# Optimization experiments

Hardware: AMD Instinct MI355X
Metric: run time of the kernel (lower is better)

Reference implementation:

```python
import jax, jax.numpy as jnp
import numpy as np

B, N, E, F, FE, H = 4, 1024, 65536, 96, 32, 12
DH = F // H
EPS = 1e-3  # keras LayerNormalization default epsilon


def layer_norm(x, g, b):
    m = jnp.mean(x, axis=-1, keepdims=True)
    v = jnp.var(x, axis=-1, keepdims=True)
    return (x - m) / jnp.sqrt(v + EPS) * g + b


def setup_inputs() -> dict:
    key = jax.random.key(0)
    ks = jax.random.split(key, 14)
    s = lambda d: 1.0 / np.sqrt(d)
    return {
        "nodes": jax.random.normal(ks[0], (B, N, F), jnp.float32),
        "edge_features": jax.random.normal(ks[1], (B, E, FE), jnp.float32),
        "distance": jax.random.uniform(ks[2], (B, E, 1), jnp.float32),
        "edges": jax.random.randint(ks[3], (B, E, 2), 0, N, jnp.int32),
        # message MLP: Dense(2F+FE -> F) + GELU + LayerNorm
        "Wm": jax.random.normal(ks[4], (2 * F + FE, F), jnp.float32) * s(2 * F + FE),
        "bm": jnp.zeros((F,), jnp.float32),
        "g1": jnp.ones((F,), jnp.float32),
        "b1": jnp.zeros((F,), jnp.float32),
        # gated multi-head self-attention over concat([nodes, aggregated]) (2F -> F)
        "Wq": jax.random.normal(ks[5], (2 * F, F), jnp.float32) * s(2 * F),
        "bq": jnp.zeros((F,), jnp.float32),
        "Wk": jax.random.normal(ks[6], (2 * F, F), jnp.float32) * s(2 * F),
        "bk": jnp.zeros((F,), jnp.float32),
        "Wv": jax.random.normal(ks[7], (2 * F, F), jnp.float32) * s(2 * F),
        "bv": jnp.zeros((F,), jnp.float32),
        "Wg": jax.random.normal(ks[8], (2 * F, F), jnp.float32) * s(2 * F),
        "bg": jnp.zeros((F,), jnp.float32),
        "Wo": jax.random.normal(ks[9], (F, F), jnp.float32) * s(F),
        "bo": jnp.zeros((F,), jnp.float32),
        "g2": jnp.ones((F,), jnp.float32),
        "b2": jnp.zeros((F,), jnp.float32),
        # learnable gaussian edge-weight params
        "sigma": jnp.full((1,), 0.005, jnp.float32),
        "beta": jnp.full((1,), 4.0, jnp.float32),
    }


def reference(nodes, edge_features, distance, edges, Wm, bm, g1, b1,
              Wq, bq, Wk, bk, Wv, bv, Wg, bg, Wo, bo, g2, b2, sigma, beta):
    # --- message: gather endpoint node features per edge ---
    gathered = jax.vmap(lambda n, e: n[e])(nodes, edges)              # [B,E,2,F]
    msg_in = jnp.concatenate([gathered.reshape(B, E, 2 * F), edge_features], axis=-1)
    messages = layer_norm(jax.nn.gelu(msg_in @ Wm + bm, approximate=False), g1, b1)  # [B,E,F]
    # --- learnable gaussian edge weighting ---
    edge_weights = jnp.exp(-((distance ** 2 / (2.0 * sigma ** 2)) ** beta))           # [B,E,1]
    weighted_messages = messages * edge_weights
    # --- scatter: per-graph segment-sum into receiver nodes (edge[:,1]) ---
    aggregated = jax.vmap(lambda m, seg: jax.ops.segment_sum(m, seg, num_segments=N))(
        weighted_messages, edges[..., 1])                             # [B,N,F]
    # --- update: gated multi-head self-attention on concat([nodes, aggregated]) ---
    x = jnp.concatenate([nodes, aggregated], axis=-1)                 # [B,N,2F]
    heads = lambda t: t.reshape(B, N, H, DH).transpose(0, 2, 1, 3)    # [B,H,N,DH]
    q, k, v = heads(x @ Wq + bq), heads(x @ Wk + bk), heads(x @ Wv + bv)
    gate = heads(jax.nn.sigmoid(x @ Wg + bg))
    attn = jax.nn.softmax(jnp.einsum("bhqd,bhkd->bhqk", q, k) / jnp.sqrt(jnp.float32(DH)), axis=-1)
    out = (jnp.einsum("bhqk,bhkd->bhqd", attn, v) * gate).transpose(0, 2, 1, 3).reshape(B, N, F)
    out = out @ Wo + bo
    updated_nodes = layer_norm(jax.nn.gelu(out, approximate=False), g2, b2)
    return (updated_nodes, weighted_messages, distance, edges)
```

## Files before the change

kernel.cpp:

```cpp
#include <hip/hip_runtime.h>
#include <math.h>

#define Bn 4
#define Nn 1024
#define En 65536
#define Fn 96
#define FEn 32
#define Hn 12

#define OUT_UPD  0
#define OUT_WM   393216LL
#define OUT_DIST 25559040LL
#define OUT_EDGE 25821184LL

#define WS_AGG  0
#define WS_Q    393216
#define WS_K    786432
#define WS_V    1179648
#define WS_G    1572864
#define WS_AO   1966080
#define WS_LIST 2359296
#define WS_LW   2424832
#define WS_CNT  2490368

#define MSG_NWAVES 1024

__device__ __forceinline__ float gelu_exact(float x) {
    return 0.5f * x * (1.0f + erff(x * 0.70710678118654752f));
}

__device__ __forceinline__ void zero_wm_chunk(int c, const float* __restrict__ dist,
                                              const float* __restrict__ sigma,
                                              const float* __restrict__ beta,
                                              float* __restrict__ out_wm,
                                              int tid, int nthr, int* s_act) {
    if (tid < 256) {
        int ge = c * 256 + tid;
        float d = dist[ge];
        float sg = sigma[0], bt = beta[0];
        float t = d * d / (2.0f * sg * sg);
        s_act[tid] = (powf(t, bt) < 90.0f) ? 1 : 0;
    }
    __syncthreads();
    const float4 z = make_float4(0.f, 0.f, 0.f, 0.f);
    float4* wm4 = (float4*)out_wm + (size_t)c * 6144;
    for (int p = tid; p < 6144; p += nthr) {
        if (!s_act[p / 24]) wm4[p] = z;
    }
}

__global__ void zero_kernel(float* __restrict__ agg, int* __restrict__ gcnt) {
    int i = blockIdx.x * 256 + threadIdx.x;
    const float4 z = make_float4(0.f, 0.f, 0.f, 0.f);
    float4* p = (float4*)agg;
    p[i] = z;
    p[i + 49152] = z;
    if (i == 0) gcnt[0] = 0;
}

__global__ __launch_bounds__(1024) void scan_kernel(
        const float* __restrict__ dist, const int* __restrict__ edges,
        const float* __restrict__ sigma, const float* __restrict__ beta,
        float* __restrict__ out_dist, float* __restrict__ out_edges,
        int* __restrict__ glist, float* __restrict__ gw,
        int* __restrict__ gcnt) {
    __shared__ int wcnt[16], wbase[16], blkbase;
    int tid = threadIdx.x;
    int lane = tid & 63, wv = tid >> 6;
    int ge = blockIdx.x * 1024 + tid;
    float d = dist[ge];
    out_dist[ge] = d;
    int e0 = edges[2 * ge], e1 = edges[2 * ge + 1];
    *(float2*)&out_edges[2 * ge] = make_float2((float)e0, (float)e1);
    float sg = sigma[0], bt = beta[0];
    float t  = d * d / (2.0f * sg * sg);
    float tp = powf(t, bt);
    bool active = (tp < 90.0f);
    float w = active ? expf(-tp) : 0.0f;

    unsigned long long mask = __ballot(active);
    int lp = __popcll(mask & ((1ull << lane) - 1ull));
    if (lane == 0) wcnt[wv] = __popcll(mask);
    __syncthreads();
    if (tid == 0) {
        int a = 0;
        #pragma unroll
        for (int i = 0; i < 16; ++i) { wbase[i] = a; a += wcnt[i]; }
        blkbase = a ? atomicAdd(gcnt, a) : 0;
    }
    __syncthreads();
    if (active) {
        int pos = blkbase + wbase[wv] + lp;
        if (pos < 65536) { glist[pos] = ge; gw[pos] = w; }
    }
}

__global__ __launch_bounds__(256) void msg_kernel(
        const int* __restrict__ glist, const float* __restrict__ gw,
        const int* __restrict__ gcnt, const int* __restrict__ edges,
        const float* __restrict__ nodes, const float* __restrict__ ef,
        const float* __restrict__ Wm, const float* __restrict__ bm,
        const float* __restrict__ g1, const float* __restrict__ b1,
        float* __restrict__ out_wm, float* __restrict__ agg) {
    __shared__ float sin_s[4][4][232];
    int tid = threadIdx.x;
    int lane = tid & 63, wv = tid >> 6;
    int count = gcnt[0];
    if (count > 65536) count = 65536;
    int c2 = 64 + (lane & 31);
    int wid = blockIdx.x * 4 + wv;

    for (int base = wid * 4; base < count; base += MSG_NWAVES * 4) {
        int   gei[4];
        float wgt[4];
        bool  val[4];
        #pragma unroll
        for (int e = 0; e < 4; ++e) {
            int ai = base + e;
            val[e] = (ai < count);
            int as = val[e] ? ai : base;
            gei[e] = glist[as];
            wgt[e] = val[e] ? gw[ai] : 0.0f;
        }
        #pragma unroll
        for (int e = 0; e < 4; ++e) {
            int g = gei[e];
            int b = g >> 16;
            int e0 = edges[2 * g], e1 = edges[2 * g + 1];
            const float* n0 = nodes + ((size_t)b * Nn + e0) * 96;
            const float* n1 = nodes + ((size_t)b * Nn + e1) * 96;
            const float* ep = ef + (size_t)g * 32;
            #pragma unroll
            for (int ii = 0; ii < 4; ++ii) {
                int i = ii * 64 + lane;
                if (i < 224) {
                    float v = (i < 96) ? n0[i] : (i < 192) ? n1[i - 96] : ep[i - 192];
                    sin_s[wv][e][i] = v;
                }
            }
        }
        float acc[4][2];
        #pragma unroll
        for (int e = 0; e < 4; ++e) { acc[e][0] = bm[lane]; acc[e][1] = bm[c2]; }
        #pragma unroll 8
        for (int i = 0; i < 224; ++i) {
            float w1 = Wm[i * 96 + lane];
            float w2 = Wm[i * 96 + c2];
            #pragma unroll
            for (int e = 0; e < 4; ++e) {
                float a = sin_s[wv][e][i];
                acc[e][0] = fmaf(a, w1, acc[e][0]);
                acc[e][1] = fmaf(a, w2, acc[e][1]);
            }
        }
        #pragma unroll
        for (int e = 0; e < 4; ++e) {
            if (!val[e]) continue;
            float y1 = gelu_exact(acc[e][0]);
            float y2 = gelu_exact(acc[e][1]);
            float c2v = (lane < 32) ? y2 : 0.0f;
            float sum  = y1 + c2v;
            float sum2 = y1 * y1 + c2v * c2v;
            #pragma unroll
            for (int off = 1; off < 64; off <<= 1) {
                sum  += __shfl_xor(sum, off);
                sum2 += __shfl_xor(sum2, off);
            }
            float mean = sum * (1.0f / 96.0f);
            float var  = sum2 * (1.0f / 96.0f) - mean * mean;
            float rs   = rsqrtf(var + 1e-3f);
            int g = gei[e];
            int b = g >> 16;
            int e1 = edges[2 * g + 1];
            float* aggp = agg + ((size_t)b * Nn + e1) * 96;
            float* wmp  = out_wm + (size_t)g * 96;
            float o1 = ((y1 - mean) * rs * g1[lane] + b1[lane]) * wgt[e];
            wmp[lane] = o1;
            atomicAdd(&aggp[lane], o1);
            if (lane < 32) {
                float o2 = ((y2 - mean) * rs * g1[c2] + b1[c2]) * wgt[e];
                wmp[c2] = o2;
                atomicAdd(&aggp[c2], o2);
            }
        }
    }
}

__global__ void proj_kernel(const float* __restrict__ nodes, const float* __restrict__ agg,
                            const float* __restrict__ Wq, const float* __restrict__ bq,
                            const float* __restrict__ Wk, const float* __restrict__ bk,
                            const float* __restrict__ Wv, const float* __restrict__ bv,
                            const float* __restrict__ Wg, const float* __restrict__ bg,
                            float* __restrict__ qo, float* __restrict__ ko,
                            float* __restrict__ vo, float* __restrict__ go,
                            const float* __restrict__ dist, const float* __restrict__ sigma,
                            const float* __restrict__ beta, float* __restrict__ out_wm) {
    __shared__ float xs[32][200];
    __shared__ float Wt[64 * 96];
    __shared__ int s_act[256];
    int tid = threadIdx.x;
    int m = blockIdx.y;
    if (m == 0) {
        zero_wm_chunk(768 + blockIdx.x, dist, sigma, beta, out_wm, tid, 256, s_act);
    }
    const float* W    = (m == 0) ? Wq : (m == 1) ? Wk : (m == 2) ? Wv : Wg;
    const float* bias = (m == 0) ? bq : (m == 1) ? bk : (m == 2) ? bv : bg;
    float* outp       = (m == 0) ? qo : (m == 1) ? ko : (m == 2) ? vo : go;
    int row0 = blockIdx.x * 32;
    int b = row0 >> 10, n0 = row0 & 1023;
    for (int i = tid; i < 32 * 192; i += 256) {
        int r = i / 192, k = i % 192;
        size_t row = row0 + r;
        xs[r][k] = (k < 96) ? nodes[row * 96 + k] : agg[row * 96 + (k - 96)];
    }
    int rg = tid >> 4;
    int cg = tid & 15;
    float acc[12];
    #pragma unroll
    for (int c = 0; c < 12; ++c) acc[c] = 0.0f;
    for (int kc = 0; kc < 3; ++kc) {
        __syncthreads();
        {
            float4* Wt4 = (float4*)Wt;
            const float4* Wg4 = (const float4*)(W + kc * 64 * 96);
            for (int i = tid; i < 1536; i += 256) Wt4[i] = Wg4[i];
        }
        __syncthreads();
        #pragma unroll 4
        for (int k = 0; k < 64; ++k) {
            float a0 = xs[rg * 2 + 0][kc * 64 + k];
            float a1 = xs[rg * 2 + 1][kc * 64 + k];
            #pragma unroll
            for (int c = 0; c < 6; ++c) {
                float wv_ = Wt[k * 96 + cg * 6 + c];
                acc[c]     = fmaf(a0, wv_, acc[c]);
                acc[6 + c] = fmaf(a1, wv_, acc[6 + c]);
            }
        }
    }
    #pragma unroll
    for (int i = 0; i < 2; ++i) {
        #pragma unroll
        for (int c = 0; c < 6; ++c) {
            int col = cg * 6 + c;
            float v = acc[i * 6 + c] + bias[col];
            if (m == 3) v = 1.0f / (1.0f + expf(-v));
            xs[rg * 2 + i][col] = v;
        }
    }
    __syncthreads();
    float4* out4 = (float4*)outp;
    for (int j = tid; j < 768; j += 256) {
        int h = j >> 6, idx = j & 63;
        int r = idx >> 1, half = idx & 1;
        float4 v = *(const float4*)&xs[r][h * 8 + half * 4];
        out4[(((size_t)b * Hn + h) * Nn + n0) * 2 + idx] = v;
    }
}

__global__ __launch_bounds__(512, 6) void attn_kernel(
        const float* __restrict__ qp, const float* __restrict__ kp,
        const float* __restrict__ vp, const float* __restrict__ gp,
        float* __restrict__ ao,
        const float* __restrict__ dist, const float* __restrict__ sigma,
        const float* __restrict__ beta, float* __restrict__ out_wm) {
    __shared__ float sl[512];
    __shared__ float sacc[512][9];
    __shared__ int s_act[256];
    int tid = threadIdx.x;
    zero_wm_chunk(blockIdx.y * 16 + blockIdx.x, dist, sigma, beta, out_wm, tid, 512, s_act);
    int bh = blockIdx.y;
    int lane = tid & 63;
    int w = __builtin_amdgcn_readfirstlane(tid >> 6);
    int n = blockIdx.x * 64 + lane;
    size_t hb = (size_t)bh * (Nn * 8);
    size_t qoff = hb + (size_t)n * 8;

    const float scale = 0.35355339059327376f;
    float4 q0 = *(const float4*)&qp[qoff];
    float4 q1 = *(const float4*)&qp[qoff + 4];
    q0.x *= scale; q0.y *= scale; q0.z *= scale; q0.w *= scale;
    q1.x *= scale; q1.y *= scale; q1.z *= scale; q1.w *= scale;

    const float4* kc4 = (const float4*)(kp + hb) + (size_t)w * 256;
    const float4* vc4 = (const float4*)(vp + hb) + (size_t)w * 256;

    float l = 0.0f;
    float a0 = 0, a1 = 0, a2 = 0, a3 = 0, a4 = 0, a5 = 0, a6 = 0, a7 = 0;
    for (int g = 0; g < 32; ++g) {
        float4 T[8];
        #pragma unroll
        for (int i = 0; i < 8; ++i) T[i] = kc4[g * 8 + i];
        float s[4];
        #pragma unroll
        for (int jj = 0; jj < 4; ++jj) {
            float4 k0 = T[jj * 2], k1 = T[jj * 2 + 1];
            s[jj] = q0.x * k0.x + q0.y * k0.y + q0.z * k0.z + q0.w * k0.w +
                    q1.x * k1.x + q1.y * k1.y + q1.z * k1.z + q1.w * k1.w;
        }
        #pragma unroll
        for (int i = 0; i < 8; ++i) T[i] = vc4[g * 8 + i];
        float p[4];
        #pragma unroll
        for (int jj = 0; jj < 4; ++jj) p[jj] = __expf(s[jj]);
        l += (p[0] + p[1]) + (p[2] + p[3]);
        #pragma unroll
        for (int jj = 0; jj < 4; ++jj) {
            float4 v0 = T[jj * 2], v1 = T[jj * 2 + 1];
            a0 = fmaf(p[jj], v0.x, a0);  a1 = fmaf(p[jj], v0.y, a1);
            a2 = fmaf(p[jj], v0.z, a2);  a3 = fmaf(p[jj], v0.w, a3);
            a4 = fmaf(p[jj], v1.x, a4);  a5 = fmaf(p[jj], v1.y, a5);
            a6 = fmaf(p[jj], v1.z, a6);  a7 = fmaf(p[jj], v1.w, a7);
        }
    }
    sl[tid] = l;
    sacc[tid][0] = a0; sacc[tid][1] = a1; sacc[tid][2] = a2; sacc[tid][3] = a3;
    sacc[tid][4] = a4; sacc[tid][5] = a5; sacc[tid][6] = a6; sacc[tid][7] = a7;
    __syncthreads();
    if (tid < 64) {
        float L = 0.0f;
        float o[8] = {0, 0, 0, 0, 0, 0, 0, 0};
        #pragma unroll
        for (int i = 0; i < 8; ++i) {
            L += sl[tid + 64 * i];
            #pragma unroll
            for (int d = 0; d < 8; ++d)
                o[d] += sacc[tid + 64 * i][d];
        }
        float invL = 1.0f / L;
        float4 g0 = *(const float4*)&gp[qoff];
        float4 g1v = *(const float4*)&gp[qoff + 4];
        float4 r0 = make_float4(o[0] * invL * g0.x, o[1] * invL * g0.y,
                                o[2] * invL * g0.z, o[3] * invL * g0.w);
        float4 r1 = make_float4(o[4] * invL * g1v.x, o[5] * invL * g1v.y,
                                o[6] * invL * g1v.z, o[7] * invL * g1v.w);
        *(float4*)&ao[qoff] = r0;
        *(float4*)&ao[qoff + 4] = r1;
    }
}

__global__ __launch_bounds__(512) void out_kernel(
        const float* __restrict__ ao, const float* __restrict__ Wo,
        const float* __restrict__ bo, const float* __restrict__ g2,
        const float* __restrict__ b2, float* __restrict__ out0,
        const float* __restrict__ dist, const float* __restrict__ sigma,
        const float* __restrict__ beta, float* __restrict__ out_wm) {
    __shared__ float Wsh[96 * 96];
    __shared__ float as_[32][104];
    __shared__ int s_act[256];
    int tid = threadIdx.x;
    zero_wm_chunk(896 + blockIdx.x, dist, sigma, beta, out_wm, tid, 512, s_act);
    int row0 = blockIdx.x * 32;
    int b = row0 >> 10, n0 = row0 & 1023;
    {
        float4* W4 = (float4*)Wsh;
        const float4* Wg4 = (const float4*)Wo;
        for (int i = tid; i < 2304; i += 512) W4[i] = Wg4[i];
    }
    const float4* ao4 = (const float4*)ao;
    for (int j = tid; j < 768; j += 512) {
        int h = j >> 6, idx = j & 63;
        int r = idx >> 1, half = idx & 1;
        float4 v = ao4[(((size_t)b * Hn + h) * Nn + n0) * 2 + idx];
        *(float4*)&as_[r][h * 8 + half * 4] = v;
    }
    __syncthreads();
    int r = tid >> 4, cg = tid & 15;
    float acc[6];
    #pragma unroll
    for (int c = 0; c < 6; ++c) acc[c] = 0.0f;
    for (int k = 0; k < 96; ++k) {
        float a = as_[r][k];
        #pragma unroll
        for (int c = 0; c < 6; ++c)
            acc[c] = fmaf(a, Wsh[k * 96 + cg * 6 + c], acc[c]);
    }
    float yv[6];
    float sum = 0.0f, sum2 = 0.0f;
    #pragma unroll
    for (int c = 0; c < 6; ++c) {
        float t = acc[c] + bo[cg * 6 + c];
        float g = gelu_exact(t);
        yv[c] = g;
        sum += g; sum2 += g * g;
    }
    #pragma unroll
    for (int off = 1; off < 16; off <<= 1) {
        sum  += __shfl_xor(sum, off);
        sum2 += __shfl_xor(sum2, off);
    }
    float mean = sum * (1.0f / 96.0f);
    float var  = sum2 * (1.0f / 96.0f) - mean * mean;
    float rs   = rsqrtf(var + 1e-3f);
    size_t row = row0 + r;
    #pragma unroll
    for (int c = 0; c < 6; ++c)
        out0[row * 96 + cg * 6 + c] = (yv[c] - mean) * rs * g2[cg * 6 + c] + b2[cg * 6 + c];
}

extern "C" void kernel_launch(void* const* d_in, const int* in_sizes, int n_in,
                              void* d_out, int out_size, void* d_ws, size_t ws_size,
                              hipStream_t stream) {
    const float* nodes = (const float*)d_in[0];
    const float* ef    = (const float*)d_in[1];
    const float* dist  = (const float*)d_in[2];
    const int*   edges = (const int*)d_in[3];
    const float* Wm = (const float*)d_in[4];
    const float* bm = (const float*)d_in[5];
    const float* g1 = (const float*)d_in[6];
    const float* b1 = (const float*)d_in[7];
    const float* Wq = (const float*)d_in[8];
    const float* bq = (const float*)d_in[9];
    const float* Wk = (const float*)d_in[10];
    const float* bk = (const float*)d_in[11];
    const float* Wv = (const float*)d_in[12];
    const float* bv = (const float*)d_in[13];
    const float* Wg = (const float*)d_in[14];
    const float* bg = (const float*)d_in[15];
    const float* Wo = (const float*)d_in[16];
    const float* bo = (const float*)d_in[17];
    const float* g2 = (const float*)d_in[18];
    const float* b2 = (const float*)d_in[19];
    const float* sigma = (const float*)d_in[20];
    const float* beta  = (const float*)d_in[21];

    float* out = (float*)d_out;
    float* ws  = (float*)d_ws;

    float* agg  = ws + WS_AGG;
    float* qb   = ws + WS_Q;
    float* kb   = ws + WS_K;
    float* vb   = ws + WS_V;
    float* gwb  = ws + WS_G;
    float* aob  = ws + WS_AO;
    int*   glist = (int*)(ws + WS_LIST);
    float* glw   = ws + WS_LW;
    int*   gcnt  = (int*)(ws + WS_CNT);

    zero_kernel<<<192, 256, 0, stream>>>(agg, gcnt);

    scan_kernel<<<Bn * En / 1024, 1024, 0, stream>>>(
        dist, edges, sigma, beta, out + OUT_DIST, out + OUT_EDGE, glist, glw, gcnt);

    msg_kernel<<<256, 256, 0, stream>>>(
        glist, glw, gcnt, edges, nodes, ef, Wm, bm, g1, b1, out + OUT_WM, agg);

    dim3 gp_(128, 4);
    proj_kernel<<<gp_, 256, 0, stream>>>(
        nodes, agg, Wq, bq, Wk, bk, Wv, bv, Wg, bg, qb, kb, vb, gwb,
        dist, sigma, beta, out + OUT_WM);

    dim3 ga(16, Bn * Hn);
    attn_kernel<<<ga, 512, 0, stream>>>(qb, kb, vb, gwb, aob,
                                        dist, sigma, beta, out + OUT_WM);

    out_kernel<<<Bn * Nn / 32, 512, 0, stream>>>(aob, Wo, bo, g2, b2, out + OUT_UPD,
                                                 dist, sigma, beta, out + OUT_WM);
}
```

Measured before the change: 113.9 us.

## Rewrite attention kernel with bf16 MFMA and LDS-staged K/V

Replaces the scalar fp32 per-query attention loop with a bf16 MFMA formulation. K and a transposed V are converted to bf16 and staged in shared memory, with a row of ones appended to V so the softmax denominator comes out of the same MFMA. Each wave processes 16 queries over 32-key chunks, passing probabilities through LDS between the two MFMAs. This cuts the FP32 ALU work and the redundant global K/V reads, at the cost of bf16 precision in scores and probabilities, no max subtraction, and a per-block staging of the full K/V into LDS.

```diff
diff --git a/kernel.cpp b/kernel.cpp
--- a/kernel.cpp
+++ b/kernel.cpp
@@ -25,8 +25,17 @@
 
 #define MSG_NWAVES 1024
 
+typedef __attribute__((ext_vector_type(8))) short bf16x8;
+typedef __attribute__((ext_vector_type(4))) float f32x4;
+
 __device__ __forceinline__ float gelu_exact(float x) {
     return 0.5f * x * (1.0f + erff(x * 0.70710678118654752f));
+}
+
+__device__ __forceinline__ unsigned cvtpk_bf16(float lo, float hi) {
+    unsigned r;
+    asm("v_cvt_pk_bf16_f32 %0, %1, %2" : "=v"(r) : "v"(lo), "v"(hi));
+    return r;
 }
 
 __device__ __forceinline__ void zero_wm_chunk(int c, const float* __restrict__ dist,
@@ -258,84 +267,92 @@
     }
 }
 
-__global__ __launch_bounds__(512, 6) void attn_kernel(
+__global__ __launch_bounds__(256, 4) void attn_kernel(
         const float* __restrict__ qp, const float* __restrict__ kp,
         const float* __restrict__ vp, const float* __restrict__ gp,
         float* __restrict__ ao,
         const float* __restrict__ dist, const float* __restrict__ sigma,
         const float* __restrict__ beta, float* __restrict__ out_wm) {
-    __shared__ float sl[512];
-    __shared__ float sacc[512][9];
+    __shared__ __align__(16) unsigned short K_s[1024][8];
+    __shared__ __align__(16) unsigned short Vt_s[9][1032];
+    __shared__ __align__(16) unsigned short P_s[4][16][32];
     __shared__ int s_act[256];
     int tid = threadIdx.x;
-    zero_wm_chunk(blockIdx.y * 16 + blockIdx.x, dist, sigma, beta, out_wm, tid, 512, s_act);
+    zero_wm_chunk(blockIdx.y * 16 + blockIdx.x, dist, sigma, beta, out_wm, tid, 256, s_act);
+
     int bh = blockIdx.y;
-    int lane = tid & 63;
-    int w = __builtin_amdgcn_readfirstlane(tid >> 6);
-    int n = blockIdx.x * 64 + lane;
+    int lane = tid & 63, wv = tid >> 6;
     size_t hb = (size_t)bh * (Nn * 8);
-    size_t qoff = hb + (size_t)n * 8;
+    const float* kc = kp + hb;
+    const float* vc = vp + hb;
+
+    {
+        const float2* k2 = (const float2*)kc;
+        unsigned* kw = (unsigned*)&K_s[0][0];
+        for (int i = tid; i < 4096; i += 256) {
+            float2 v = k2[i];
+            kw[i] = cvtpk_bf16(v.x, v.y);
+        }
+    }
+    for (int i = tid; i < 8192; i += 256) {
+        float v = vc[i];
+        int k = i >> 3, n = i & 7;
+        Vt_s[n][k] = (unsigned short)cvtpk_bf16(v, v);
+    }
+    {
+        unsigned* ow = (unsigned*)&Vt_s[8][0];
+        for (int i = tid; i < 516; i += 256) ow[i] = 0x3F803F80u;
+    }
 
     const float scale = 0.35355339059327376f;
-    float4 q0 = *(const float4*)&qp[qoff];
-    float4 q1 = *(const float4*)&qp[qoff + 4];
-    q0.x *= scale; q0.y *= scale; q0.z *= scale; q0.w *= scale;
-    q1.x *= scale; q1.y *= scale; q1.z *= scale; q1.w *= scale;
-
-    const float4* kc4 = (const float4*)(kp + hb) + (size_t)w * 256;
-    const float4* vc4 = (const float4*)(vp + hb) + (size_t)w * 256;
-
-    float l = 0.0f;
-    float a0 = 0, a1 = 0, a2 = 0, a3 = 0, a4 = 0, a5 = 0, a6 = 0, a7 = 0;
-    for (int g = 0; g < 32; ++g) {
-        float4 T[8];
-        #pragma unroll
-        for (int i = 0; i < 8; ++i) T[i] = kc4[g * 8 + i];
-        float s[4];
-        #pragma unroll
-        for (int jj = 0; jj < 4; ++jj) {
-            float4 k0 = T[jj * 2], k1 = T[jj * 2 + 1];
-            s[jj] = q0.x * k0.x + q0.y * k0.y + q0.z * k0.z + q0.w * k0.w +
-                    q1.x * k1.x + q1.y * k1.y + q1.z * k1.z + q1.w * k1.w;
-        }
-        #pragma unroll
-        for (int i = 0; i < 8; ++i) T[i] = vc4[g * 8 + i];
-        float p[4];
-        #pragma unroll
-        for (int jj = 0; jj < 4; ++jj) p[jj] = __expf(s[jj]);
-        l += (p[0] + p[1]) + (p[2] + p[3]);
-        #pragma unroll
-        for (int jj = 0; jj < 4; ++jj) {
-            float4 v0 = T[jj * 2], v1 = T[jj * 2 + 1];
-            a0 = fmaf(p[jj], v0.x, a0);  a1 = fmaf(p[jj], v0.y, a1);
-            a2 = fmaf(p[jj], v0.z, a2);  a3 = fmaf(p[jj], v0.w, a3);
-            a4 = fmaf(p[jj], v1.x, a4);  a5 = fmaf(p[jj], v1.y, a5);
-            a6 = fmaf(p[jj], v1.z, a6);  a7 = fmaf(p[jj], v1.w, a7);
-        }
-    }
-    sl[tid] = l;
-    sacc[tid][0] = a0; sacc[tid][1] = a1; sacc[tid][2] = a2; sacc[tid][3] = a3;
-    sacc[tid][4] = a4; sacc[tid][5] = a5; sacc[tid][6] = a6; sacc[tid][7] = a7;
-    __syncthreads();
-    if (tid < 64) {
-        float L = 0.0f;
-        float o[8] = {0, 0, 0, 0, 0, 0, 0, 0};
-        #pragma unroll
-        for (int i = 0; i < 8; ++i) {
-            L += sl[tid + 64 * i];
-            #pragma unroll
-            for (int d = 0; d < 8; ++d)
-                o[d] += sacc[tid + 64 * i][d];
-        }
-        float invL = 1.0f / L;
-        float4 g0 = *(const float4*)&gp[qoff];
-        float4 g1v = *(const float4*)&gp[qoff + 4];
-        float4 r0 = make_float4(o[0] * invL * g0.x, o[1] * invL * g0.y,
-                                o[2] * invL * g0.z, o[3] * invL * g0.w);
-        float4 r1 = make_float4(o[4] * invL * g1v.x, o[5] * invL * g1v.y,
-                                o[6] * invL * g1v.z, o[7] * invL * g1v.w);
-        *(float4*)&ao[qoff] = r0;
-        *(float4*)&ao[qoff + 4] = r1;
+    int qbase = blockIdx.x * 64 + wv * 16;
+    bf16x8 aq = {0, 0, 0, 0, 0, 0, 0, 0};
+    if (lane < 16) {
+        const float* qr = qp + hb + (size_t)(qbase + lane) * 8;
+        float4 qa = *(const float4*)qr;
+        float4 qb2 = *(const float4*)(qr + 4);
+        union { unsigned u[4]; bf16x8 v; } U;
+        U.u[0] = cvtpk_bf16(qa.x * scale, qa.y * scale);
+        U.u[1] = cvtpk_bf16(qa.z * scale, qa.w * scale);
+        U.u[2] = cvtpk_bf16(qb2.x * scale, qb2.y * scale);
+        U.u[3] = cvtpk_bf16(qb2.z * scale, qb2.w * scale);
+        aq = U.v;
+    }
+    __syncthreads();
+
+    const bf16x8 zero8 = {0, 0, 0, 0, 0, 0, 0, 0};
+    const f32x4 zero4 = {0.f, 0.f, 0.f, 0.f};
+    f32x4 o = zero4;
+    int n16 = lane & 15, grp = lane >> 4;
+    for (int c = 0; c < 32; ++c) {
+        bf16x8 bk0 = zero8, bk1 = zero8;
+        if (lane < 16) {
+            bk0 = *(const bf16x8*)&K_s[c * 32 + lane][0];
+            bk1 = *(const bf16x8*)&K_s[c * 32 + 16 + lane][0];
+        }
+        f32x4 s0 = __builtin_amdgcn_mfma_f32_16x16x32_bf16(aq, bk0, zero4, 0, 0, 0);
+        f32x4 s1 = __builtin_amdgcn_mfma_f32_16x16x32_bf16(aq, bk1, zero4, 0, 0, 0);
+        #pragma unroll
+        for (int r = 0; r < 4; ++r) {
+            unsigned pk = cvtpk_bf16(__expf(s0[r]), __expf(s1[r]));
+            int row = grp * 4 + r;
+            P_s[wv][row][n16]      = (unsigned short)pk;
+            P_s[wv][row][16 + n16] = (unsigned short)(pk >> 16);
+        }
+        bf16x8 pa = *(const bf16x8*)&P_s[wv][n16][grp * 8];
+        bf16x8 bv = zero8;
+        if (n16 <= 8) bv = *(const bf16x8*)&Vt_s[n16][c * 32 + grp * 8];
+        o = __builtin_amdgcn_mfma_f32_16x16x32_bf16(pa, bv, o, 0, 0, 0);
+    }
+
+    #pragma unroll
+    for (int r = 0; r < 4; ++r) {
+        float L = __shfl(o[r], (lane & 48) | 8);
+        if (n16 < 8) {
+            int q = qbase + grp * 4 + r;
+            size_t off = hb + (size_t)q * 8 + n16;
+            ao[off] = o[r] / L * gp[off];
+        }
     }
 }
 
@@ -451,7 +468,7 @@
         dist, sigma, beta, out + OUT_WM);
 
     dim3 ga(16, Bn * Hn);
-    attn_kernel<<<ga, 512, 0, stream>>>(qb, kb, vb, gwb, aob,
+    attn_kernel<<<ga, 256, 0, stream>>>(qb, kb, vb, gwb, aob,
                                         dist, sigma, beta, out + OUT_WM);
 
     out_kernel<<<Bn * Nn / 32, 512, 0, stream>>>(aob, Wo, bo, g2, b2, out + OUT_UPD,
```

New measurement: 112.2 us. About the same (-1.5%).
